# Optimization experiments

Measured on AMD Instinct MI355X. Metric: run time of the kernel, lower is better.

Reference implementation:

```python
import jax, jax.numpy as jnp
import numpy as np

B, L, E, H = 4, 4096, 1024, 16
D = E // H  # head_dim = 64
EPS = 1e-4


def setup_inputs() -> dict:
    key = jax.random.key(0)
    k1, k2, k3 = jax.random.split(key, 3)
    x = jax.random.normal(k1, (B, L, E), dtype=jnp.float32)
    W_qkv = jax.random.normal(k2, (E, 3 * E), dtype=jnp.float32) * (1.0 / np.sqrt(E))
    b_qkv = jnp.zeros((3 * E,), dtype=jnp.float32)
    W_out = jax.random.normal(k3, (E, E), dtype=jnp.float32) * (1.0 / np.sqrt(E))
    b_out = jnp.zeros((E,), dtype=jnp.float32)
    return {"x": x, "W_qkv": W_qkv, "b_qkv": b_qkv, "W_out": W_out, "b_out": b_out}


def reference(x, W_qkv, b_qkv, W_out, b_out):
    Bb, Ll, Ee = x.shape
    qkv = x @ W_qkv + b_qkv                      # [B, L, 3E]
    q, k, v = jnp.split(qkv, 3, axis=-1)
    # [B, H, L, D]
    q = q.reshape(Bb, Ll, H, D).transpose(0, 2, 1, 3)
    k = k.reshape(Bb, Ll, H, D).transpose(0, 2, 1, 3)
    v = v.reshape(Bb, Ll, H, D).transpose(0, 2, 1, 3)

    positions = jnp.arange(Ll, dtype=jnp.float32).reshape(1, 1, Ll, 1)
    cos_w = jnp.cos(jnp.pi / 2 * positions / Ll)
    sin_w = jnp.sin(jnp.pi / 2 * positions / Ll)

    q_prime = jax.nn.relu(q)
    k_prime = jax.nn.relu(k)

    q_cos, q_sin = q_prime * cos_w, q_prime * sin_w
    k_cos, k_sin = k_prime * cos_w, k_prime * sin_w

    # O(L) linear attention: accumulate KV outer products per head
    kv_cos = jnp.einsum('bhld,bhle->bhde', k_cos, v)      # [B,H,D,D]
    kv_sin = jnp.einsum('bhld,bhle->bhde', k_sin, v)
    context = (jnp.einsum('bhld,bhde->bhle', q_cos, kv_cos)
               + jnp.einsum('bhld,bhde->bhle', q_sin, kv_sin))  # [B,H,L,D]

    k_cos_sum = k_cos.sum(axis=2)                          # [B,H,D]
    k_sin_sum = k_sin.sum(axis=2)
    norm = (jnp.einsum('bhld,bhd->bhl', q_cos, k_cos_sum)
            + jnp.einsum('bhld,bhd->bhl', q_sin, k_sin_sum))

    output = context / (norm[..., None] + EPS)
    output = output.transpose(0, 2, 1, 3).reshape(Bb, Ll, Ee)
    return output @ W_out + b_out
```

## Files before the change

### kernel.cpp

```cpp
#include <hip/hip_runtime.h>
#include <hip/hip_bf16.h>
#include <cstdint>
#include <cstddef>

#define BB 4
#define LL 4096
#define HH 16
#define M1 16384
#define E3 3072
#define EE 1024
#define ANGC 3.8349519697141029e-4f
#define EPSC 1e-4f

typedef __attribute__((ext_vector_type(8))) short bf16x8;
typedef __attribute__((ext_vector_type(4))) float f32x4;
typedef __attribute__((ext_vector_type(8))) unsigned short us8;

static __device__ __forceinline__ float bf2f(unsigned short u) {
  union { unsigned int i; float f; } a; a.i = ((unsigned int)u) << 16; return a.f;
}
static __device__ __forceinline__ unsigned short f2bf(float x) {
  union { float f; unsigned int i; } a; a.f = x;
  unsigned int r = a.i + 0x7FFFu + ((a.i >> 16) & 1u);
  return (unsigned short)(r >> 16);
}
static __device__ __forceinline__ void gload16(const void* g, void* l) {
  __builtin_amdgcn_global_load_lds((const __attribute__((address_space(1))) void*)g,
                                   (__attribute__((address_space(3))) void*)l, 16, 0, 0);
}

#define BAR()   asm volatile("s_barrier" ::: "memory")
#define VMC4()  asm volatile("s_waitcnt vmcnt(4)" ::: "memory")
#define VMC0()  asm volatile("s_waitcnt vmcnt(0)" ::: "memory")
#define PRIO1() __builtin_amdgcn_s_setprio(1)
#define PRIO0() __builtin_amdgcn_s_setprio(0)

__global__ __launch_bounds__(256) void k_cvt_bf16(const float* __restrict__ src,
                                                  unsigned short* __restrict__ dst, int n8) {
  int i = blockIdx.x * 256 + threadIdx.x;
  if (i >= n8) return;
  const float4* s = (const float4*)src + (size_t)i * 2;
  float4 a = s[0], b = s[1];
  us8 o;
  o[0]=f2bf(a.x); o[1]=f2bf(a.y); o[2]=f2bf(a.z); o[3]=f2bf(a.w);
  o[4]=f2bf(b.x); o[5]=f2bf(b.y); o[6]=f2bf(b.z); o[7]=f2bf(b.w);
  *(us8*)(dst + (size_t)i * 8) = o;
}

__global__ __launch_bounds__(256) void k_transpose_bf16(const float* __restrict__ src,
                                                        unsigned short* __restrict__ dst,
                                                        int R, int C) {
  __shared__ float tile[32][33];
  int c0 = blockIdx.x * 32, r0 = blockIdx.y * 32;
  int tx = threadIdx.x & 31, ty = threadIdx.x >> 5;
#pragma unroll
  for (int k = 0; k < 4; ++k)
    tile[ty + 8*k][tx] = src[(size_t)(r0 + ty + 8*k) * C + c0 + tx];
  __syncthreads();
#pragma unroll
  for (int k = 0; k < 4; ++k)
    dst[(size_t)(c0 + ty + 8*k) * R + r0 + tx] = f2bf(tile[tx][ty + 8*k]);
}


static __device__ __forceinline__ bf16x8 rdfrag(const char* base, int row, int ck) {
  return *(const bf16x8*)(base + row * 128 + (((ck) ^ ((row) & 7)) << 4));
}

static __device__ __forceinline__ void stage_half(const unsigned short* __restrict__ M, int K,
                                                  int rowbase, int half, int kt,
                                                  char* bufbase, int tid) {
  const int rr = tid >> 3, cc = tid & 7;
  char* d = bufbase + half * 16384 + tid * 16;
  const int r0 = half * 128 + rr, r1 = r0 + 64;
  gload16(M + (size_t)(rowbase + r0) * K + kt + ((cc ^ (r0 & 7)) << 3), d);
  gload16(M + (size_t)(rowbase + r1) * K + kt + ((cc ^ (r1 & 7)) << 3), d + 8192);
}

#define PH_FIRST(AbP, BbP, AR)                                                  \
  do {                                                                          \
    _Pragma("unroll")                                                           \
    for (int n = 0; n < 4; ++n) {                                               \
      const int br = wc * 64 + n * 16 + lr;                                     \
      bF[n][0] = rdfrag((BbP), br, lg);                                         \
      bF[n][1] = rdfrag((BbP), br, 4 + lg);                                     \
    }                                                                           \
    AR[0][0] = rdfrag((AbP), wr * 128 + lr, lg);                                \
    AR[0][1] = rdfrag((AbP), wr * 128 + lr, 4 + lg);                            \
    AR[1][0] = rdfrag((AbP), wr * 128 + 16 + lr, lg);                           \
    AR[1][1] = rdfrag((AbP), wr * 128 + 16 + lr, 4 + lg);                       \
  } while (0)

#define PH_A(AbP, mb, AR)                                                       \
  do {                                                                          \
    AR[0][0] = rdfrag((AbP), wr * 128 + (mb) * 16 + lr, lg);                    \
    AR[0][1] = rdfrag((AbP), wr * 128 + (mb) * 16 + lr, 4 + lg);                \
    AR[1][0] = rdfrag((AbP), wr * 128 + (mb) * 16 + 16 + lr, lg);               \
    AR[1][1] = rdfrag((AbP), wr * 128 + (mb) * 16 + 16 + lr, 4 + lg);           \
  } while (0)

#define MMA16(mb, AR)                                                           \
  do {                                                                          \
    _Pragma("unroll")                                                           \
    for (int kk = 0; kk < 2; ++kk) {                                            \
      _Pragma("unroll")                                                         \
      for (int n = 0; n < 4; ++n) {                                             \
        acc[(mb)][n] = __builtin_amdgcn_mfma_f32_16x16x32_bf16(                 \
            AR[0][kk], bF[n][kk], acc[(mb)][n], 0, 0, 0);                       \
        acc[(mb) + 1][n] = __builtin_amdgcn_mfma_f32_16x16x32_bf16(             \
            AR[1][kk], bF[n][kk], acc[(mb) + 1][n], 0, 0, 0);                   \
      }                                                                         \
    }                                                                           \
  } while (0)

template<int MODE>
__global__ __launch_bounds__(512, 2) void k_gemm256(const unsigned short* __restrict__ A,
                                                    const unsigned short* __restrict__ Bt,
                                                    const float* __restrict__ bias,
                                                    void* __restrict__ Cout,
                                                    int N, int K) {
  __shared__ __align__(16) unsigned short lds[4][16384];
  const int tid = threadIdx.x;
  const int wid = tid >> 6, lane = tid & 63;
  const int lr = lane & 15, lg = lane >> 4;
  const int wr = wid >> 2, wc = wid & 3;

  const int nx = gridDim.x;
  const int rawbid = blockIdx.y * nx + blockIdx.x;
  const int xcd = rawbid & 7, s = rawbid >> 3;
  const int g = s >> 5, r = s & 31;
  const int bm = (xcd * 8 + (r & 7)) * 256;
  const int bn = (g * 4 + (r >> 3)) * 256;

  char* LA0 = (char*)&lds[0][0];
  char* LB0 = (char*)&lds[1][0];
  char* LA1 = (char*)&lds[2][0];
  char* LB1 = (char*)&lds[3][0];

  f32x4 acc[8][4] = {};
  bf16x8 bF[4][2], aF[2][2], aG[2][2];

  const int NT = K >> 6, NI = NT >> 1;

  stage_half(A,  K, bm, 0, 0,  LA0, tid);
  stage_half(A,  K, bm, 1, 0,  LA0, tid);
  stage_half(Bt, K, bn, 0, 0,  LB0, tid);
  stage_half(Bt, K, bn, 1, 0,  LB0, tid);
  stage_half(Bt, K, bn, 0, 64, LB1, tid);
  stage_half(Bt, K, bn, 1, 64, LB1, tid);
  VMC4();
  BAR();

  for (int it = 0; it < NI; ++it) {
    const int kt1 = (2*it + 1) << 6;
    const int kt2 = (2*it + 2) << 6;
    const int kt3 = (2*it + 3) << 6;
    const bool s2 = kt2 < K, s3 = kt3 < K;

    PH_FIRST(LA0, LB0, aF);
    stage_half(A, K, bm, 0, kt1, LA1, tid);
    BAR(); PRIO1(); MMA16(0, aF); PRIO0(); BAR();

    PH_A(LA0, 2, aG);
    stage_half(A, K, bm, 1, kt1, LA1, tid);
    if (s2) stage_half(Bt, K, bn, 0, kt2, LB0, tid);
    BAR(); PRIO1(); MMA16(2, aG); PRIO0(); BAR();

    PH_A(LA0, 4, aF);
    if (s2) stage_half(Bt, K, bn, 1, kt2, LB0, tid);
    BAR(); PRIO1(); MMA16(4, aF); PRIO0(); BAR();

    PH_A(LA0, 6, aG);
    BAR(); PRIO1(); MMA16(6, aG); PRIO0();
    if (it == NI - 1) { VMC0(); } else { VMC4(); }
    BAR();

    PH_FIRST(LA1, LB1, aF);
    if (s2) stage_half(A, K, bm, 0, kt2, LA0, tid);
    BAR(); PRIO1(); MMA16(0, aF); PRIO0(); BAR();

    PH_A(LA1, 2, aG);
    if (s2) stage_half(A, K, bm, 1, kt2, LA0, tid);
    if (s3) stage_half(Bt, K, bn, 0, kt3, LB1, tid);
    BAR(); PRIO1(); MMA16(2, aG); PRIO0(); BAR();

    PH_A(LA1, 4, aF);
    if (s3) stage_half(Bt, K, bn, 1, kt3, LB1, tid);
    BAR(); PRIO1(); MMA16(4, aF); PRIO0(); BAR();

    PH_A(LA1, 6, aG);
    BAR(); PRIO1(); MMA16(6, aG); PRIO0();
    VMC4();
    BAR();
  }

  {
    float* strip = (float*)((char*)&lds[0][0] + wid * 16384);
    float bias_v[4]; bool relu_v[4];
#pragma unroll
    for (int n = 0; n < 4; ++n) {
      int col = bn + wc*64 + n*16 + lr;
      bias_v[n] = bias[col];
      relu_v[n] = (MODE == 0) && (col < 2048);
    }
#pragma unroll
    for (int m = 0; m < 8; ++m) {
#pragma unroll
      for (int n = 0; n < 4; ++n)
#pragma unroll
        for (int j = 0; j < 4; ++j) {
          float v = acc[m][n][j] + bias_v[n];
          if (relu_v[n]) v = fmaxf(v, 0.0f);
          strip[(lg*4 + j)*68 + n*16 + lr] = v;
        }
#pragma unroll
      for (int itr = 0; itr < 4; ++itr) {
        int ch = itr*64 + lane;
        int row = ch >> 4, cg = ch & 15;
        float4 v = *(const float4*)(strip + row*68 + cg*4);
        size_t base = (size_t)(bm + wr*128 + m*16 + row) * N + bn + wc*64 + cg*4;
        if (MODE == 0) {
          ushort4 o;
          o.x = f2bf(v.x); o.y = f2bf(v.y); o.z = f2bf(v.z); o.w = f2bf(v.w);
          *(ushort4*)((unsigned short*)Cout + base) = o;
        } else {
          *(float4*)((float*)Cout + base) = v;
        }
      }
    }
  }
}

__global__ __launch_bounds__(256) void k_stage2(const unsigned short* __restrict__ qkv,
                                                float* __restrict__ kvb,
                                                float* __restrict__ ksumb) {
  __shared__ __align__(16) unsigned short kcT[4096];
  __shared__ __align__(16) unsigned short ksT[4096];
  __shared__ __align__(16) unsigned short vT [4096];
  const int tid = threadIdx.x;
  const int head = blockIdx.y;
  const int b = head >> 4, h = head & 15;
  const int lane = tid & 63, wid = tid >> 6;
  const int lr = lane & 15, lg = lane >> 4;
  const int mt = wid >> 1, eh = wid & 1;
  const int lp = tid & 31;
  const int piece = tid >> 5;

  f32x4 acc[2][4] = {};
  float ksacc = 0.0f;
  const int mtk = tid >> 6, dk = tid & 63;
  const size_t qbase = (size_t)b * LL * E3;

  for (int sc = 0; sc < 4; ++sc) {
    const int lbase = blockIdx.x * 256 + sc * 64;
    __syncthreads();
    {
      const int l0 = 2 * lp;
      const int p0 = lbase + l0;
      float s0, c0, s1, c1;
      __sincosf((float)p0 * ANGC, &s0, &c0);
      __sincosf((float)(p0 + 1) * ANGC, &s1, &c1);
      const unsigned short* kp = qkv + qbase + (size_t)p0 * E3 + 1024 + h*64 + piece*8;
      us8 kr0 = *(const us8*)kp;
      us8 kr1 = *(const us8*)(kp + E3);
      us8 vr0 = *(const us8*)(kp + 1024);
      us8 vr1 = *(const us8*)(kp + 1024 + E3);
#pragma unroll
      for (int i = 0; i < 8; ++i) {
        int d = piece*8 + i;
        float ka = bf2f(kr0[i]), kb = bf2f(kr1[i]);
        unsigned int kcp = (unsigned int)f2bf(c0*ka) | ((unsigned int)f2bf(c1*kb) << 16);
        unsigned int ksp = (unsigned int)f2bf(s0*ka) | ((unsigned int)f2bf(s1*kb) << 16);
        unsigned int vp  = (unsigned int)vr0[i] | ((unsigned int)vr1[i] << 16);
        int off = d*128 + ((((l0 >> 3) ^ (d & 7))) << 4) + (l0 & 7) * 2;
        *(unsigned int*)((char*)kcT + off) = kcp;
        *(unsigned int*)((char*)ksT + off) = ksp;
        *(unsigned int*)((char*)vT  + off) = vp;
      }
    }
    __syncthreads();
    if (tid < 128) {
      const unsigned short* basep = mtk ? ksT : kcT;
      float sum = 0.0f;
#pragma unroll
      for (int cch = 0; cch < 8; ++cch) {
        us8 r = *(const us8*)((const char*)basep + dk*128 + ((cch ^ (dk & 7)) << 4));
#pragma unroll
        for (int i = 0; i < 8; ++i) sum += bf2f(r[i]);
      }
      ksacc += sum;
    }
    {
      const unsigned short* kT = mt ? ksT : kcT;
      bf16x8 af[2][2], bf[2][4];
#pragma unroll
      for (int kk = 0; kk < 2; ++kk) {
#pragma unroll
        for (int m = 0; m < 2; ++m) {
          int e = eh*32 + m*16 + lr;
          af[kk][m] = *(const bf16x8*)((const char*)vT + e*128 + ((((kk*4)+lg) ^ (e & 7)) << 4));
        }
#pragma unroll
        for (int n = 0; n < 4; ++n) {
          int d = n*16 + lr;
          bf[kk][n] = *(const bf16x8*)((const char*)kT + d*128 + ((((kk*4)+lg) ^ (d & 7)) << 4));
        }
      }
#pragma unroll
      for (int kk = 0; kk < 2; ++kk)
#pragma unroll
        for (int m = 0; m < 2; ++m)
#pragma unroll
          for (int n = 0; n < 4; ++n)
            acc[m][n] = __builtin_amdgcn_mfma_f32_16x16x32_bf16(af[kk][m], bf[kk][n], acc[m][n], 0, 0, 0);
    }
  }
  float* dst = kvb + (size_t)head * 8192 + mt * 4096;
#pragma unroll
  for (int m = 0; m < 2; ++m)
#pragma unroll
    for (int n = 0; n < 4; ++n)
#pragma unroll
      for (int j = 0; j < 4; ++j) {
        int e = eh*32 + m*16 + lg*4 + j;
        int d = n*16 + lr;
        atomicAdd(&dst[e*64 + d], acc[m][n][j]);
      }
  if (tid < 128) atomicAdd(&ksumb[head*128 + mtk*64 + dk], ksacc);
}

__global__ __launch_bounds__(256) void k_stage3(const unsigned short* __restrict__ qkv,
                                                const float* __restrict__ kvb,
                                                const float* __restrict__ ksumb,
                                                unsigned short* __restrict__ att) {
  __shared__ __align__(16) unsigned short Bl[144 * 64];
  const int tid = threadIdx.x;
  const int head = blockIdx.y;
  const int b = head >> 4, h = head & 15;
  const int l0 = blockIdx.x * 128;
  const int lane = tid & 63, w = tid >> 6;
  const int lr = lane & 15, lg = lane >> 4;

  {
    int c = tid >> 1, half = tid & 1;
    const float* src = kvb + (size_t)head * 8192 + (c >> 6) * 4096 + (c & 63) * 64 + half * 32;
    float fv[32];
#pragma unroll
    for (int q = 0; q < 8; ++q) *(float4*)(fv + q*4) = *(const float4*)(src + q*4);
#pragma unroll
    for (int q2 = 0; q2 < 4; ++q2) {
      us8 o;
#pragma unroll
      for (int i = 0; i < 8; ++i) o[i] = f2bf(fv[q2*8 + i]);
      int chunk = half*4 + q2;
      *(us8*)((char*)Bl + c*128 + ((chunk ^ (c & 7)) << 4)) = o;
    }
    if (tid < 16) {
      int cc = 128 + (tid >> 3), q = tid & 7;
      const float* s2 = ksumb + head*128 + (tid >> 3)*64 + q*8;
      us8 o;
#pragma unroll
      for (int i = 0; i < 8; ++i) o[i] = f2bf(s2[i]);
      *(us8*)((char*)Bl + cc*128 + ((q ^ (cc & 7)) << 4)) = o;
    } else if (tid < 128) {
      int idx = tid - 16;
      int cc = 130 + (idx >> 3), q = idx & 7;
      us8 o = {0,0,0,0,0,0,0,0};
      *(us8*)((char*)Bl + cc*128 + ((q ^ (cc & 7)) << 4)) = o;
    }
  }
  __syncthreads();

  f32x4 acc[2][9] = {};
  bf16x8 af[2][2];
  const size_t qrow0 = (size_t)(b * LL + l0 + w * 32);
#pragma unroll
  for (int kk = 0; kk < 2; ++kk)
#pragma unroll
    for (int m = 0; m < 2; ++m)
      af[m][kk] = *(const bf16x8*)(qkv + (qrow0 + m*16 + lr) * E3 + h*64 + kk*32 + lg*8);
#pragma unroll
  for (int kk = 0; kk < 2; ++kk)
#pragma unroll
    for (int n = 0; n < 9; ++n) {
      int cc = n*16 + lr;
      bf16x8 bb = *(const bf16x8*)((const char*)Bl + cc*128 + ((((kk*4)+lg) ^ (cc & 7)) << 4));
#pragma unroll
      for (int m = 0; m < 2; ++m)
        acc[m][n] = __builtin_amdgcn_mfma_f32_16x16x32_bf16(af[m][kk], bb, acc[m][n], 0, 0, 0);
    }

  __syncthreads();
  unsigned short* strip = (unsigned short*)Bl + w * 2048;
#pragma unroll
  for (int m = 0; m < 2; ++m)
#pragma unroll
    for (int j = 0; j < 4; ++j) {
      int rloc = m*16 + lg*4 + j;
      int pos = l0 + w*32 + rloc;
      float s_, c_;
      __sincosf((float)pos * ANGC, &s_, &c_);
      float nc = __shfl(acc[m][8][j], lane & 48, 64);
      float ns = __shfl(acc[m][8][j], (lane & 48) | 1, 64);
      float rn = 1.0f / (c_ * nc + s_ * ns + EPSC);
#pragma unroll
      for (int n = 0; n < 4; ++n) {
        float ctx = (c_ * acc[m][n][j] + s_ * acc[m][n+4][j]) * rn;
        strip[rloc*64 + n*16 + lr] = f2bf(ctx);
      }
    }
  __syncthreads();
#pragma unroll
  for (int p = 0; p < 4; ++p) {
    int ch = p*64 + lane;
    int row = ch >> 3, piece = ch & 7;
    us8 o = *(const us8*)(strip + row*64 + piece*8);
    *(us8*)(att + (size_t)(b*LL + l0 + w*32 + row) * EE + h*64 + piece*8) = o;
  }
}

extern "C" void kernel_launch(void* const* d_in, const int* in_sizes, int n_in,
                              void* d_out, int out_size, void* d_ws, size_t ws_size,
                              hipStream_t stream) {
  const float* x     = (const float*)d_in[0];
  const float* W_qkv = (const float*)d_in[1];
  const float* b_qkv = (const float*)d_in[2];
  const float* W_out = (const float*)d_in[3];
  const float* b_out = (const float*)d_in[4];

  char* w = (char*)d_ws;
  unsigned short* xb  = (unsigned short*)(w);
  unsigned short* qkv = (unsigned short*)(w + 33554432);
  unsigned short* WqT = (unsigned short*)(w + 134217728);
  unsigned short* WoT = (unsigned short*)(w + 140509184);
  float* kvb   = (float*)(w + 142606336);
  float* ksum  = (float*)(w + 144703488);
  unsigned short* att = xb;

  hipMemsetAsync(kvb, 0, 2097152 + 32768, stream);
  k_cvt_bf16<<<8192, 256, 0, stream>>>(x, xb, 2097152);
  k_transpose_bf16<<<dim3(96, 32), 256, 0, stream>>>(W_qkv, WqT, 1024, 3072);
  k_transpose_bf16<<<dim3(32, 32), 256, 0, stream>>>(W_out, WoT, 1024, 1024);
  k_gemm256<0><<<dim3(12, 64), 512, 0, stream>>>(xb, WqT, b_qkv, (void*)qkv, 3072, 1024);
  k_stage2<<<dim3(16, 64), 256, 0, stream>>>(qkv, kvb, ksum);
  k_stage3<<<dim3(32, 64), 256, 0, stream>>>(qkv, kvb, ksum, att);
  k_gemm256<1><<<dim3(4, 64), 512, 0, stream>>>(att, WoT, b_out, d_out, 1024, 1024);
}
```

Measured before the change: 234.0 us.

## Drop trailing GEMM barriers, hoist staging addresses, spread B-tile loads

The GEMM main loop no longer issues the second barrier after each MFMA phase; it keeps only the barrier before each MMA. Global-load offsets for the A and B tiles are now computed once before the loop instead of inside every staging call. The B-tile prefetch is moved to later phases so each phase issues a more even share of loads. The goal is less barrier stall and less address arithmetic in the hot loop. The risk is an LDS race if any wave still reads a buffer that another wave has started overwriting.

Measured after the change: 237.1 us. Within noise of the previous version (+1.3%).

```diff
diff --git a/kernel.cpp b/kernel.cpp
--- a/kernel.cpp
+++ b/kernel.cpp
@@ -67,14 +67,10 @@
   return *(const bf16x8*)(base + row * 128 + (((ck) ^ ((row) & 7)) << 4));
 }
 
-static __device__ __forceinline__ void stage_half(const unsigned short* __restrict__ M, int K,
-                                                  int rowbase, int half, int kt,
-                                                  char* bufbase, int tid) {
-  const int rr = tid >> 3, cc = tid & 7;
-  char* d = bufbase + half * 16384 + tid * 16;
-  const int r0 = half * 128 + rr, r1 = r0 + 64;
-  gload16(M + (size_t)(rowbase + r0) * K + kt + ((cc ^ (r0 & 7)) << 3), d);
-  gload16(M + (size_t)(rowbase + r1) * K + kt + ((cc ^ (r1 & 7)) << 3), d + 8192);
+static __device__ __forceinline__ void stage2h(const unsigned short* __restrict__ base,
+                                               size_t off, size_t rowK64, char* ldst) {
+  gload16(base + off, ldst);
+  gload16(base + off + rowK64, ldst + 8192);
 }
 
 #define PH_FIRST(AbP, BbP, AR)                                                  \
@@ -140,14 +136,20 @@
   f32x4 acc[8][4] = {};
   bf16x8 bF[4][2], aF[2][2], aG[2][2];
 
+  const int rr = tid >> 3, cc = tid & 7;
+  const size_t rowK64 = (size_t)64 * K, rowK128 = (size_t)128 * K;
+  const size_t aoff = (size_t)(bm + rr) * K + ((cc ^ (rr & 7)) << 3);
+  const size_t boff = (size_t)(bn + rr) * K + ((cc ^ (rr & 7)) << 3);
+  char* const dst16 = (char*)0 + tid * 16;
+
+#define STAGE_A(h, kt, L) stage2h(A,  aoff + (h) * rowK128 + (kt), rowK64, (L) + (h) * 16384 + tid * 16)
+#define STAGE_B(h, kt, L) stage2h(Bt, boff + (h) * rowK128 + (kt), rowK64, (L) + (h) * 16384 + tid * 16)
+
   const int NT = K >> 6, NI = NT >> 1;
 
-  stage_half(A,  K, bm, 0, 0,  LA0, tid);
-  stage_half(A,  K, bm, 1, 0,  LA0, tid);
-  stage_half(Bt, K, bn, 0, 0,  LB0, tid);
-  stage_half(Bt, K, bn, 1, 0,  LB0, tid);
-  stage_half(Bt, K, bn, 0, 64, LB1, tid);
-  stage_half(Bt, K, bn, 1, 64, LB1, tid);
+  STAGE_A(0, 0, LA0); STAGE_A(1, 0, LA0);
+  STAGE_B(0, 0, LB0); STAGE_B(1, 0, LB0);
+  STAGE_B(0, 64, LB1); STAGE_B(1, 64, LB1);
   VMC4();
   BAR();
 
@@ -158,41 +160,43 @@
     const bool s2 = kt2 < K, s3 = kt3 < K;
 
     PH_FIRST(LA0, LB0, aF);
-    stage_half(A, K, bm, 0, kt1, LA1, tid);
-    BAR(); PRIO1(); MMA16(0, aF); PRIO0(); BAR();
+    STAGE_A(0, kt1, LA1);
+    BAR(); PRIO1(); MMA16(0, aF); PRIO0();
 
     PH_A(LA0, 2, aG);
-    stage_half(A, K, bm, 1, kt1, LA1, tid);
-    if (s2) stage_half(Bt, K, bn, 0, kt2, LB0, tid);
-    BAR(); PRIO1(); MMA16(2, aG); PRIO0(); BAR();
+    STAGE_A(1, kt1, LA1);
+    BAR(); PRIO1(); MMA16(2, aG); PRIO0();
 
     PH_A(LA0, 4, aF);
-    if (s2) stage_half(Bt, K, bn, 1, kt2, LB0, tid);
-    BAR(); PRIO1(); MMA16(4, aF); PRIO0(); BAR();
+    if (s2) STAGE_B(0, kt2, LB0);
+    BAR(); PRIO1(); MMA16(4, aF); PRIO0();
 
     PH_A(LA0, 6, aG);
+    if (s2) STAGE_B(1, kt2, LB0);
     BAR(); PRIO1(); MMA16(6, aG); PRIO0();
     if (it == NI - 1) { VMC0(); } else { VMC4(); }
     BAR();
 
     PH_FIRST(LA1, LB1, aF);
-    if (s2) stage_half(A, K, bm, 0, kt2, LA0, tid);
-    BAR(); PRIO1(); MMA16(0, aF); PRIO0(); BAR();
+    if (s2) STAGE_A(0, kt2, LA0);
+    BAR(); PRIO1(); MMA16(0, aF); PRIO0();
 
     PH_A(LA1, 2, aG);
-    if (s2) stage_half(A, K, bm, 1, kt2, LA0, tid);
-    if (s3) stage_half(Bt, K, bn, 0, kt3, LB1, tid);
-    BAR(); PRIO1(); MMA16(2, aG); PRIO0(); BAR();
+    if (s2) STAGE_A(1, kt2, LA0);
+    BAR(); PRIO1(); MMA16(2, aG); PRIO0();
 
     PH_A(LA1, 4, aF);
-    if (s3) stage_half(Bt, K, bn, 1, kt3, LB1, tid);
-    BAR(); PRIO1(); MMA16(4, aF); PRIO0(); BAR();
+    if (s3) STAGE_B(0, kt3, LB1);
+    BAR(); PRIO1(); MMA16(4, aF); PRIO0();
 
     PH_A(LA1, 6, aG);
+    if (s3) STAGE_B(1, kt3, LB1);
     BAR(); PRIO1(); MMA16(6, aG); PRIO0();
     VMC4();
     BAR();
   }
+#undef STAGE_A
+#undef STAGE_B
 
   {
     float* strip = (float*)((char*)&lds[0][0] + wid * 16384);
@@ -229,6 +233,7 @@
       }
     }
   }
+  (void)dst16;
 }
 
 __global__ __launch_bounds__(256) void k_stage2(const unsigned short* __restrict__ qkv,
```
